# Kernel optimization log

Measured on AMD Instinct MI355X. Metric: run time of the kernel, lower is better.

## Reference

```python
import jax, jax.numpy as jnp
import numpy as np

KH, KW = 3, 3  # window_size[1], window_size[2]
FILTERS = 64
CHANNELS = 32
K = KH * KW * CHANNELS


def _extract_patches_valid(x, kh, kw):
    # TF tf.image.extract_patches ordering: (row_offset, col_offset, channel)
    B, H, W, C = x.shape
    Ho, Wo = H - kh + 1, W - kw + 1
    cols = [x[:, i:i + Ho, j:j + Wo, :] for i in range(kh) for j in range(kw)]
    return jnp.concatenate(cols, axis=-1)  # (B, Ho, Wo, kh*kw*C)


def setup_inputs() -> dict:
    key = jax.random.key(0)
    kx, kw = jax.random.split(key)
    x = jax.random.normal(kx, (8, 32, 32, CHANNELS), dtype=jnp.float32)
    # learned weight per __init__: shape (1, 1, 1, K, filters), random_normal init
    w = jax.random.normal(kw, (1, 1, 1, K, FILTERS), dtype=jnp.float32) * 0.05
    return {"x": x, "w": w}


def reference(x, w):
    # patches: (B, Ho, Wo, K)
    patches = _extract_patches_valid(x, KH, KW)
    # broadcast-add against weights: (B, Ho, Wo, K, filters)
    s = patches[..., None] + w[0, 0, 0]  # w[0,0,0]: (K, filters)
    # tropical conv: max over patch axis minus min over patch axis
    return jnp.max(s, axis=3) - jnp.min(s, axis=3)  # (B, Ho, Wo, filters)
```

## Files before the change

kernel.cpp:

```cpp
#include <hip/hip_runtime.h>


#define C_IN 32
#define NF 64
#define H_OUT 30
#define W_OUT 30
#define W_IN 32

__global__ __launch_bounds__(256) void tropconv_kernel(
    const float* __restrict__ x,
    const float* __restrict__ w,
    float* __restrict__ out) {
    const int bho = blockIdx.x;
    const int b = bho / H_OUT;
    const int ho = bho - b * H_OUT;
    const int tid = threadIdx.x;
    const int lane = tid & 63;
    const int wave = tid >> 6;

    __shared__ float xs[3 * W_IN * C_IN];

    const float4* __restrict__ xsrc =
        (const float4*)(x + (size_t)(b * 32 + ho) * (W_IN * C_IN));
    float4* xdst = (float4*)xs;
    #pragma unroll
    for (int r = 0; r < 3; ++r) {
        xdst[tid + r * 256] = xsrc[tid + r * 256];
    }
    __syncthreads();

    float mx[8], mn[8];
    #pragma unroll
    for (int t = 0; t < 8; ++t) { mx[t] = -INFINITY; mn[t] = INFINITY; }

    float wreg[C_IN];
    for (int ij = 0; ij < 9; ++ij) {
        const int i = ij / 3;
        const int j = ij - i * 3;

        const float* __restrict__ wp = w + (size_t)(ij * C_IN) * NF + lane;
        #pragma unroll
        for (int c = 0; c < C_IN; ++c) wreg[c] = wp[c * NF];

        const float* xrow = xs + i * (W_IN * C_IN) + j * C_IN;

        #pragma unroll
        for (int t = 0; t < 8; ++t) {
            const int wo = wave + 4 * t;
            if (wo < W_OUT) {
                const float4* __restrict__ pp = (const float4*)(xrow + wo * C_IN);
                #pragma unroll
                for (int c4 = 0; c4 < C_IN / 4; ++c4) {
                    float4 p = pp[c4];
                    float s0 = p.x + wreg[4 * c4 + 0];
                    float s1 = p.y + wreg[4 * c4 + 1];
                    float s2 = p.z + wreg[4 * c4 + 2];
                    float s3 = p.w + wreg[4 * c4 + 3];
                    mx[t] = fmaxf(fmaxf(mx[t], fmaxf(s0, s1)), fmaxf(s2, s3));
                    mn[t] = fminf(fminf(mn[t], fminf(s0, s1)), fminf(s2, s3));
                }
            }
        }
    }

    #pragma unroll
    for (int t = 0; t < 8; ++t) {
        const int wo = wave + 4 * t;
        if (wo < W_OUT) {
            out[((size_t)bho * W_OUT + wo) * NF + lane] = mx[t] - mn[t];
        }
    }
}

extern "C" void kernel_launch(void* const* d_in, const int* in_sizes, int n_in,
                              void* d_out, int out_size, void* d_ws, size_t ws_size,
                              hipStream_t stream) {
    const float* x = (const float*)d_in[0];
    const float* w = (const float*)d_in[1];
    float* out = (float*)d_out;

    dim3 grid(8 * H_OUT);
    dim3 block(256);
    tropconv_kernel<<<grid, block, 0, stream>>>(x, w, out);
}
```

Measured before the change: 75.88 us.

## Split output row into column quarters and channel slices across waves

The grid grows fourfold so that each block handles eight output columns of one row instead of the full row. Within a block, each wave now covers an 8-channel slice for all pixels rather than a subset of pixels over all channels, and partial max/min results are combined through shared memory. The goal is more blocks to fill the GPU's compute units and fewer weight registers per thread. The cost is an extra shared-memory reduction, a second barrier, and redundant loading of halo columns.

After: 64.89 us. -14.5%, faster.

```diff
diff --git a/kernel.cpp b/kernel.cpp
--- a/kernel.cpp
+++ b/kernel.cpp
@@ -11,21 +11,33 @@
     const float* __restrict__ x,
     const float* __restrict__ w,
     float* __restrict__ out) {
-    const int bho = blockIdx.x;
+    const int bx = blockIdx.x;
+    const int q = bx & 3;
+    const int bho = bx >> 2;
     const int b = bho / H_OUT;
     const int ho = bho - b * H_OUT;
     const int tid = threadIdx.x;
     const int lane = tid & 63;
     const int wave = tid >> 6;
 
-    __shared__ float xs[3 * W_IN * C_IN];
+    const int col0 = q * 8;
+    const int npx = (q == 3) ? 6 : 8;
+    const int ncols = (q == 3) ? 8 : 10;
 
-    const float4* __restrict__ xsrc =
-        (const float4*)(x + (size_t)(b * 32 + ho) * (W_IN * C_IN));
-    float4* xdst = (float4*)xs;
-    #pragma unroll
-    for (int r = 0; r < 3; ++r) {
-        xdst[tid + r * 256] = xsrc[tid + r * 256];
+    __shared__ float xs[3 * 10 * C_IN];
+    __shared__ float pmx[4][8][NF];
+    __shared__ float pmn[4][8][NF];
+
+    {
+        const int nf4_row = ncols * (C_IN / 4);
+        const int total_f4 = 3 * nf4_row;
+        if (tid < total_f4) {
+            const int r = tid / nf4_row;
+            const int cc = tid - r * nf4_row;
+            const float4* __restrict__ src = (const float4*)(
+                x + ((size_t)((b * 32 + ho + r) * W_IN + col0)) * C_IN);
+            ((float4*)xs)[r * 80 + cc] = src[cc];
+        }
     }
     __syncthreads();
 
@@ -33,42 +45,57 @@
     #pragma unroll
     for (int t = 0; t < 8; ++t) { mx[t] = -INFINITY; mn[t] = INFINITY; }
 
-    float wreg[C_IN];
     for (int ij = 0; ij < 9; ++ij) {
         const int i = ij / 3;
         const int j = ij - i * 3;
 
-        const float* __restrict__ wp = w + (size_t)(ij * C_IN) * NF + lane;
+        float wreg[8];
+        const float* __restrict__ wp =
+            w + ((size_t)(ij * C_IN + wave * 8)) * NF + lane;
         #pragma unroll
-        for (int c = 0; c < C_IN; ++c) wreg[c] = wp[c * NF];
-
-        const float* xrow = xs + i * (W_IN * C_IN) + j * C_IN;
+        for (int cc = 0; cc < 8; ++cc) wreg[cc] = wp[cc * NF];
 
         #pragma unroll
-        for (int t = 0; t < 8; ++t) {
-            const int wo = wave + 4 * t;
-            if (wo < W_OUT) {
-                const float4* __restrict__ pp = (const float4*)(xrow + wo * C_IN);
-                #pragma unroll
-                for (int c4 = 0; c4 < C_IN / 4; ++c4) {
-                    float4 p = pp[c4];
-                    float s0 = p.x + wreg[4 * c4 + 0];
-                    float s1 = p.y + wreg[4 * c4 + 1];
-                    float s2 = p.z + wreg[4 * c4 + 2];
-                    float s3 = p.w + wreg[4 * c4 + 3];
-                    mx[t] = fmaxf(fmaxf(mx[t], fmaxf(s0, s1)), fmaxf(s2, s3));
-                    mn[t] = fminf(fminf(mn[t], fminf(s0, s1)), fminf(s2, s3));
-                }
+        for (int px = 0; px < 8; ++px) {
+            if (px < npx) {
+                const float* __restrict__ pp =
+                    xs + (i * 10 + (px + j)) * C_IN + wave * 8;
+                float4 p0 = ((const float4*)pp)[0];
+                float4 p1 = ((const float4*)pp)[1];
+                float s0 = p0.x + wreg[0];
+                float s1 = p0.y + wreg[1];
+                float s2 = p0.z + wreg[2];
+                float s3 = p0.w + wreg[3];
+                float s4 = p1.x + wreg[4];
+                float s5 = p1.y + wreg[5];
+                float s6 = p1.z + wreg[6];
+                float s7 = p1.w + wreg[7];
+                float hi = fmaxf(fmaxf(fmaxf(s0, s1), fmaxf(s2, s3)),
+                                 fmaxf(fmaxf(s4, s5), fmaxf(s6, s7)));
+                float lo = fminf(fminf(fminf(s0, s1), fminf(s2, s3)),
+                                 fminf(fminf(s4, s5), fminf(s6, s7)));
+                mx[px] = fmaxf(mx[px], hi);
+                mn[px] = fminf(mn[px], lo);
             }
         }
     }
 
     #pragma unroll
-    for (int t = 0; t < 8; ++t) {
-        const int wo = wave + 4 * t;
-        if (wo < W_OUT) {
-            out[((size_t)bho * W_OUT + wo) * NF + lane] = mx[t] - mn[t];
-        }
+    for (int px = 0; px < 8; ++px) {
+        pmx[wave][px][lane] = mx[px];
+        pmn[wave][px][lane] = mn[px];
+    }
+    __syncthreads();
+
+    const int nout = npx * NF;
+    for (int e = tid; e < nout; e += 256) {
+        const int px = e >> 6;
+        const int f = e & 63;
+        float a = fmaxf(fmaxf(pmx[0][px][f], pmx[1][px][f]),
+                        fmaxf(pmx[2][px][f], pmx[3][px][f]));
+        float m = fminf(fminf(pmn[0][px][f], pmn[1][px][f]),
+                        fminf(pmn[2][px][f], pmn[3][px][f]));
+        out[((size_t)bho * W_OUT + (col0 + px)) * NF + f] = a - m;
     }
 }
 
@@ -79,7 +106,7 @@
     const float* w = (const float*)d_in[1];
     float* out = (float*)d_out;
 
-    dim3 grid(8 * H_OUT);
+    dim3 grid(8 * H_OUT * 4);
     dim3 block(256);
     tropconv_kernel<<<grid, block, 0, stream>>>(x, w, out);
 }
```

## Transpose weights and remap threads to pixels with wave-uniform filter groups

Applied to the files above, without the earlier changes.

Adds a small pre-kernel that transposes the weights to filter-major layout in the workspace. The main kernel now runs one 64-thread wave per block, with each lane owning one output pixel (two rows by 32 columns) and each block handling four filters. Weight reads become uniform across the wave and can be served as scalar loads, while patch data comes straight from global memory without shared-memory staging. Each lane writes a float4 of four filters. The cost is a second launch and repeated patch reads from global/L2 across the 16 filter-group blocks.

New measurement: 113.4 us. 49.5% more time.

```diff
diff --git a/kernel.cpp b/kernel.cpp
--- a/kernel.cpp
+++ b/kernel.cpp
@@ -6,69 +6,83 @@
 #define H_OUT 30
 #define W_OUT 30
 #define W_IN 32
+#define KTOT 288
 
-__global__ __launch_bounds__(256) void tropconv_kernel(
+static __device__ __forceinline__ float max3f(float a, float b, float c) {
+    return fmaxf(fmaxf(a, b), c);
+}
+static __device__ __forceinline__ float min3f(float a, float b, float c) {
+    return fminf(fminf(a, b), c);
+}
+
+__global__ __launch_bounds__(256) void transpose_w_kernel(
+    const float* __restrict__ w, float* __restrict__ wT) {
+    const int idx = blockIdx.x * 256 + threadIdx.x;
+    if (idx < KTOT * NF) {
+        const int f = idx / KTOT;
+        const int k = idx - f * KTOT;
+        wT[idx] = w[k * NF + f];
+    }
+}
+
+__global__ __launch_bounds__(64) void tropconv_kernel(
     const float* __restrict__ x,
-    const float* __restrict__ w,
+    const float* __restrict__ wT,
     float* __restrict__ out) {
-    const int bho = blockIdx.x;
-    const int b = bho / H_OUT;
-    const int ho = bho - b * H_OUT;
-    const int tid = threadIdx.x;
-    const int lane = tid & 63;
-    const int wave = tid >> 6;
+    const int bx = blockIdx.x;
+    const int fg = bx & 15;
+    const int bb = bx >> 4;
+    const int b = bb / 15;
+    const int rp = bb - b * 15;
 
-    __shared__ float xs[3 * W_IN * C_IN];
+    const int lane = threadIdx.x;
+    const int wo_raw = lane & 31;
+    const int r = lane >> 5;
+    const int row = rp * 2 + r;
+    const int wo = (wo_raw < W_OUT) ? wo_raw : (W_OUT - 1);
 
-    const float4* __restrict__ xsrc =
-        (const float4*)(x + (size_t)(b * 32 + ho) * (W_IN * C_IN));
-    float4* xdst = (float4*)xs;
+    const float* __restrict__ wt0 = wT + (size_t)(fg * 4) * KTOT;
+
+    float mx[4], mn[4];
     #pragma unroll
-    for (int r = 0; r < 3; ++r) {
-        xdst[tid + r * 256] = xsrc[tid + r * 256];
-    }
-    __syncthreads();
+    for (int fi = 0; fi < 4; ++fi) { mx[fi] = -INFINITY; mn[fi] = INFINITY; }
 
-    float mx[8], mn[8];
     #pragma unroll
-    for (int t = 0; t < 8; ++t) { mx[t] = -INFINITY; mn[t] = INFINITY; }
+    for (int i = 0; i < 3; ++i) {
+        #pragma unroll
+        for (int j = 0; j < 3; ++j) {
+            const int ij = i * 3 + j;
+            const float4* __restrict__ pp = (const float4*)(
+                x + ((size_t)((b * 32 + row + i) * W_IN + (wo + j))) * C_IN);
+            float4 p[8];
+            #pragma unroll
+            for (int c4 = 0; c4 < 8; ++c4) p[c4] = pp[c4];
 
-    float wreg[C_IN];
-    for (int ij = 0; ij < 9; ++ij) {
-        const int i = ij / 3;
-        const int j = ij - i * 3;
-
-        const float* __restrict__ wp = w + (size_t)(ij * C_IN) * NF + lane;
-        #pragma unroll
-        for (int c = 0; c < C_IN; ++c) wreg[c] = wp[c * NF];
-
-        const float* xrow = xs + i * (W_IN * C_IN) + j * C_IN;
-
-        #pragma unroll
-        for (int t = 0; t < 8; ++t) {
-            const int wo = wave + 4 * t;
-            if (wo < W_OUT) {
-                const float4* __restrict__ pp = (const float4*)(xrow + wo * C_IN);
+            #pragma unroll
+            for (int fi = 0; fi < 4; ++fi) {
+                const float* __restrict__ wr = wt0 + (size_t)fi * KTOT + ij * C_IN;
                 #pragma unroll
-                for (int c4 = 0; c4 < C_IN / 4; ++c4) {
-                    float4 p = pp[c4];
-                    float s0 = p.x + wreg[4 * c4 + 0];
-                    float s1 = p.y + wreg[4 * c4 + 1];
-                    float s2 = p.z + wreg[4 * c4 + 2];
-                    float s3 = p.w + wreg[4 * c4 + 3];
-                    mx[t] = fmaxf(fmaxf(mx[t], fmaxf(s0, s1)), fmaxf(s2, s3));
-                    mn[t] = fminf(fminf(mn[t], fminf(s0, s1)), fminf(s2, s3));
+                for (int c4 = 0; c4 < 8; ++c4) {
+                    float s0 = p[c4].x + wr[c4 * 4 + 0];
+                    float s1 = p[c4].y + wr[c4 * 4 + 1];
+                    float s2 = p[c4].z + wr[c4 * 4 + 2];
+                    float s3 = p[c4].w + wr[c4 * 4 + 3];
+                    mx[fi] = max3f(max3f(s0, s1, s2), s3, mx[fi]);
+                    mn[fi] = min3f(min3f(s0, s1, s2), s3, mn[fi]);
                 }
             }
         }
     }
 
-    #pragma unroll
-    for (int t = 0; t < 8; ++t) {
-        const int wo = wave + 4 * t;
-        if (wo < W_OUT) {
-            out[((size_t)bho * W_OUT + wo) * NF + lane] = mx[t] - mn[t];
-        }
+    if (wo_raw < W_OUT) {
+        float4 res;
+        res.x = mx[0] - mn[0];
+        res.y = mx[1] - mn[1];
+        res.z = mx[2] - mn[2];
+        res.w = mx[3] - mn[3];
+        float4* __restrict__ op = (float4*)(
+            out + ((size_t)((b * H_OUT + row) * W_OUT + wo_raw)) * NF) + fg;
+        *op = res;
     }
 }
 
@@ -78,8 +92,8 @@
     const float* x = (const float*)d_in[0];
     const float* w = (const float*)d_in[1];
     float* out = (float*)d_out;
+    float* wT = (float*)d_ws;
 
-    dim3 grid(8 * H_OUT);
-    dim3 block(256);
-    tropconv_kernel<<<grid, block, 0, stream>>>(x, w, out);
+    transpose_w_kernel<<<dim3(72), dim3(256), 0, stream>>>(w, wT);
+    tropconv_kernel<<<dim3(15 * 8 * 16), dim3(64), 0, stream>>>(x, wT, out);
 }
```
